# Kernel tuning notes

Hardware: AMD Instinct MI355X
Metric: run time of the kernel (lower is better)

Reference implementation:

```python
import jax, jax.numpy as jnp
import numpy as np
import math

B, N, DEG, C, F0, NCLS = 128, 512, 8, 128, 128, 10
E = B * N * DEG
RATIO = 0.8
K1 = math.ceil(RATIO * N)    # 410
K2 = math.ceil(RATIO * K1)   # 328
K3 = math.ceil(RATIO * K2)   # 263


def setup_inputs() -> dict:
    key = jax.random.key(0)
    ks = jax.random.split(key, 32)
    x = jax.random.normal(ks[0], (B * N, F0), jnp.float32)
    epg = N * DEG
    src_l = jax.random.randint(ks[1], (B, epg), 0, N)
    dst_l = jax.random.randint(ks[2], (B, epg), 0, N)
    off = (jnp.arange(B, dtype=jnp.int32) * N)[:, None]
    edge_src = (src_l + off).reshape(-1).astype(jnp.int32)
    edge_dst = (dst_l + off).reshape(-1).astype(jnp.int32)

    def lin(k, fi, fo):
        return jax.random.normal(k, (fi, fo), jnp.float32) / np.float32(np.sqrt(fi))

    inp = {"x": x, "edge_src": edge_src, "edge_dst": edge_dst}
    i = 3
    for s, fi in (("1", F0), ("2", C), ("3", C)):
        inp["Wroot" + s] = lin(ks[i], fi, C); i += 1
        inp["Wrel" + s] = lin(ks[i], fi, C); i += 1
        inp["brel" + s] = jnp.zeros((C,), jnp.float32)
        inp["p" + s] = jax.random.normal(ks[i], (C,), jnp.float32); i += 1
    inp["W1"] = lin(ks[i], 2 * C, 128); i += 1
    inp["b1"] = jnp.zeros((128,), jnp.float32)
    inp["W2"] = lin(ks[i], 128, 64); i += 1
    inp["b2"] = jnp.zeros((64,), jnp.float32)
    inp["W3"] = lin(ks[i], 64, NCLS); i += 1
    inp["b3"] = jnp.zeros((NCLS,), jnp.float32)
    return inp


def graph_conv(x, src, dst, emask, Wroot, Wrel, brel, num_nodes):
    # PyG GraphConv (aggr='add'): lin_rel(sum_j x_j) + lin_root(x_i)
    msg = x[src] * emask[:, None]                      # masked gather  [E, C]
    agg = jax.ops.segment_sum(msg, dst, num_segments=num_nodes)
    return agg @ Wrel + brel + x @ Wroot


def topk_pool(x, p, src, dst, emask, b, n, k):
    # score = tanh(x . p / ||p||), keep top-k nodes per graph, scale kept x by score
    score = jnp.tanh((x @ p) / jnp.linalg.norm(p))     # [b*n]
    vals, idx = jax.lax.top_k(score.reshape(b, n), k)  # [b, k]
    perm = (idx + (jnp.arange(b, dtype=idx.dtype) * n)[:, None]).reshape(-1)
    x_new = x[perm] * vals.reshape(-1, 1)
    inv = jnp.full((b * n,), -1, jnp.int32).at[perm].set(
        jnp.arange(b * k, dtype=jnp.int32))
    ns, nd = inv[src], inv[dst]
    nmask = emask * (ns >= 0) * (nd >= 0)
    return x_new, jnp.maximum(ns, 0), jnp.maximum(nd, 0), nmask


def readout(h, b, k):
    hb = h.reshape(b, k, -1)
    return jnp.concatenate([hb.max(axis=1), hb.mean(axis=1)], axis=-1)  # gmp||gap


def reference(x, edge_src, edge_dst,
              Wroot1, Wrel1, brel1, p1,
              Wroot2, Wrel2, brel2, p2,
              Wroot3, Wrel3, brel3, p3,
              W1, b1, W2, b2, W3, b3):
    emask = jnp.ones((E,), x.dtype)
    s, d = edge_src, edge_dst

    h = jax.nn.relu(graph_conv(x, s, d, emask, Wroot1, Wrel1, brel1, B * N))
    h, s, d, emask = topk_pool(h, p1, s, d, emask, B, N, K1)
    x1 = readout(h, B, K1)

    h = jax.nn.relu(graph_conv(h, s, d, emask, Wroot2, Wrel2, brel2, B * K1))
    h, s, d, emask = topk_pool(h, p2, s, d, emask, B, K1, K2)
    x2 = readout(h, B, K2)

    h = jax.nn.relu(graph_conv(h, s, d, emask, Wroot3, Wrel3, brel3, B * K2))
    h, s, d, emask = topk_pool(h, p3, s, d, emask, B, K2, K3)
    x3 = readout(h, B, K3)

    g = x1 + x2 + x3                                   # [B, 256]
    g = jax.nn.relu(g @ W1 + b1)                       # dropout is identity in eval
    g = jax.nn.relu(g @ W2 + b2)
    return jax.nn.log_softmax(g @ W3 + b3, axis=-1)    # [B, NCLS]
```

## Files before the change

### kernel.cpp

```cpp
#include <hip/hip_runtime.h>
#include <hip/hip_bf16.h>
#include <math.h>

#define B_G   128
#define N0    512
#define DEG   8
#define CCH   128
#define EPG   (N0*DEG)
#define E_TOTAL (B_G*EPG)
#define K1    410
#define K2    328
#define K3    263
#define NCLS  10

using bf16x8 = __attribute__((ext_vector_type(8))) __bf16;
using f32x4  = __attribute__((ext_vector_type(4))) float;
typedef unsigned short ushort;
typedef unsigned int uint;
typedef unsigned long long u64;

__device__ __forceinline__ ushort f2b(float f) {
    uint u = __float_as_uint(f);
    u += 0x7fffu + ((u >> 16) & 1u);
    return (ushort)(u >> 16);
}
__device__ __forceinline__ float b2f(ushort h) {
    return __uint_as_float(((uint)h) << 16);
}
__device__ __forceinline__ void split2(float v, ushort& hi, ushort& lo) {
    hi = f2b(v);
    lo = f2b(v - b2f(hi));
}
__device__ __forceinline__ uint pksplit(float v) {
    ushort h, l; split2(v, h, l);
    return (uint)h | ((uint)l << 16);
}
__device__ __forceinline__ float unpk(uint u) {
    return __uint_as_float(u << 16) + __uint_as_float(u & 0xffff0000u);
}
__device__ __forceinline__ float keyval(u64 key) {
    uint tu = (uint)(key >> 32);
    uint su = (tu & 0x80000000u) ? (tu & 0x7fffffffu) : ~tu;
    return __uint_as_float(su);
}

__global__ __launch_bounds__(512) void setup_kernel(
        const float* __restrict__ Wrel0, const float* __restrict__ Wroot0,
        const float* __restrict__ Wrel1, const float* __restrict__ Wroot1,
        const float* __restrict__ Wrel2, const float* __restrict__ Wroot2,
        ushort* __restrict__ Bph, ushort* __restrict__ Bpl,
        const int* __restrict__ es, const int* __restrict__ ed,
        int* __restrict__ indptr0, int* __restrict__ counts0, ushort* __restrict__ srclist0) {
    __shared__ uint epk[EPG];
    __shared__ int cnt[512], pref[512], curs[512];
    if (blockIdx.x < B_G) {
        int b = blockIdx.x, tid = threadIdx.x;
        cnt[tid] = 0;
        __syncthreads();
        int base = b * EPG;
        for (int i = tid; i < EPG; i += 512) {
            int s = es[base + i] & (N0 - 1);
            int d = ed[base + i] & (N0 - 1);
            epk[i] = (uint)s | ((uint)d << 16);
            atomicAdd(&cnt[d], 1);
        }
        __syncthreads();
        pref[tid] = cnt[tid];
        __syncthreads();
        for (int off = 1; off < 512; off <<= 1) {
            int v = (tid >= off) ? pref[tid - off] : 0;
            __syncthreads();
            pref[tid] += v;
            __syncthreads();
        }
        int excl = tid ? pref[tid - 1] : 0;
        indptr0[b * N0 + tid] = base + excl;
        counts0[b * N0 + tid] = cnt[tid];
        curs[tid] = excl;
        __syncthreads();
        for (int i = tid; i < EPG; i += 512) {
            uint wv = epk[i];
            int dl = wv >> 16;
            int pos = atomicAdd(&curs[dl], 1);
            srclist0[base + pos] = (ushort)(wv & 0xFFFFu);
        }
    } else {
        int i = (blockIdx.x - B_G) * 512 + threadIdx.x;
        if (i < 3 * 32768) {
            int layer = i >> 15, rem = i & 32767;
            int j = rem & 7, lane = (rem >> 3) & 63, cf = (rem >> 9) & 7, ks = rem >> 12;
            int k = ks * 32 + (lane >> 4) * 8 + j;
            int c = cf * 16 + (lane & 15);
            const float* Wrel  = layer == 0 ? Wrel0  : layer == 1 ? Wrel1  : Wrel2;
            const float* Wroot = layer == 0 ? Wroot0 : layer == 1 ? Wroot1 : Wroot2;
            float v = (k < 128) ? Wrel[k * 128 + c] : Wroot[(k - 128) * 128 + c];
            ushort hi, lo; split2(v, hi, lo);
            Bph[i] = hi; Bpl[i] = lo;
        }
    }
}

__global__ __launch_bounds__(1024) void aggregate0(
        const float* __restrict__ xf,
        const int* __restrict__ indptr, const int* __restrict__ counts,
        const ushort* __restrict__ srclist,
        uint* __restrict__ aggp) {
    extern __shared__ float slab[];
    int b = blockIdx.x >> 2, q = blockIdx.x & 3;
    int tid = threadIdx.x;
    const float4* xf4 = (const float4*)xf;
    for (int t = tid; t < N0 * 8; t += 1024) {
        int nd = t >> 3, c4 = t & 7;
        float4 u = xf4[(size_t)(b * N0 + nd) * 32 + q * 8 + c4];
        *(float4*)&slab[nd * 32 + c4 * 4] = u;
    }
    __syncthreads();
    int wave = tid >> 6, lane = tid & 63;
    int gl = lane >> 3, sub = lane & 7;
    for (int g = wave; g < N0 / 8; g += 16) {
        int d = g * 8 + gl;
        int beg = indptr[b * N0 + d];
        int cnt = counts[b * N0 + d];
        float4 acc = make_float4(0.f, 0.f, 0.f, 0.f);
        int id_next = (cnt > 0) ? (int)srclist[beg] : 0;
        for (int j = 0; j < cnt; j++) {
            int id = id_next;
            if (j + 1 < cnt) id_next = (int)srclist[beg + j + 1];
            const float4 v = *(const float4*)&slab[id * 32 + sub * 4];
            acc.x += v.x; acc.y += v.y; acc.z += v.z; acc.w += v.w;
        }
        uint4 o;
        o.x = pksplit(acc.x); o.y = pksplit(acc.y);
        o.z = pksplit(acc.z); o.w = pksplit(acc.w);
        *(uint4*)&aggp[(size_t)(b * N0 + d) * CCH + q * 32 + sub * 4] = o;
    }
}

__global__ __launch_bounds__(512, 4) void transform_mfma(
        const uint* __restrict__ aggp, const uint* __restrict__ hin,
        const float* __restrict__ rootf,
        const int* __restrict__ perm, const float* __restrict__ pval,
        const ushort* __restrict__ Bph, const ushort* __restrict__ Bpl,
        const float* __restrict__ brel, const float* __restrict__ pvec,
        uint* __restrict__ hout, float* __restrict__ score) {
    __shared__ ushort ldsBh[16384];
    __shared__ ushort ldsBl[16384];
    int tid = threadIdx.x;
    int wave = tid >> 6, lane = tid & 63;
    int r = lane & 15, kb = lane >> 4;
    int rows0 = blockIdx.x * 128 + wave * 16;
    int gid = rows0 + r;
    size_t oldrow = perm ? (size_t)perm[gid] : (size_t)gid;
    float rv = perm ? pval[gid] : 1.f;

    f32x4 acc[8];
#pragma unroll
    for (int cf = 0; cf < 8; cf++) acc[cf] = (f32x4)(0.f);

    union U16 { uint u[4]; bf16x8 v; };

#pragma unroll
    for (int half = 0; half < 2; half++) {
        if (half) __syncthreads();
#pragma unroll
        for (int i = 0; i < 4; i++) {
            int idx = tid + i * 512;
            ((uint4*)ldsBh)[idx] = ((const uint4*)(Bph + half * 16384))[idx];
            ((uint4*)ldsBl)[idx] = ((const uint4*)(Bpl + half * 16384))[idx];
        }
        __syncthreads();
#pragma unroll
        for (int ks4 = 0; ks4 < 4; ks4++) {
            U16 ah, al;
            if (half && rootf) {
                const float* R = rootf + (size_t)gid * CCH + ks4 * 32 + kb * 8;
                float4 f0 = *(const float4*)R;
                float4 f1 = *(const float4*)(R + 4);
                float c[8] = {f0.x, f0.y, f0.z, f0.w, f1.x, f1.y, f1.z, f1.w};
#pragma unroll
                for (int p2 = 0; p2 < 4; p2++) {
                    ushort h0, l0, h1, l1;
                    split2(c[2 * p2], h0, l0);
                    split2(c[2 * p2 + 1], h1, l1);
                    ah.u[p2] = (uint)h0 | ((uint)h1 << 16);
                    al.u[p2] = (uint)l0 | ((uint)l1 << 16);
                }
            } else {
                const uint* A = half ? hin : aggp;
                size_t abase = half ? oldrow * CCH : (size_t)gid * CCH;
                size_t rowbase = abase + ks4 * 32 + kb * 8;
                uint4 ua = *(const uint4*)&A[rowbase];
                uint4 ub = *(const uint4*)&A[rowbase + 4];
                if (half && perm) {
                    float c[8] = {unpk(ua.x) * rv, unpk(ua.y) * rv, unpk(ua.z) * rv,
                                  unpk(ua.w) * rv, unpk(ub.x) * rv, unpk(ub.y) * rv,
                                  unpk(ub.z) * rv, unpk(ub.w) * rv};
#pragma unroll
                    for (int p2 = 0; p2 < 4; p2++) {
                        ushort h0, l0, h1, l1;
                        split2(c[2 * p2], h0, l0);
                        split2(c[2 * p2 + 1], h1, l1);
                        ah.u[p2] = (uint)h0 | ((uint)h1 << 16);
                        al.u[p2] = (uint)l0 | ((uint)l1 << 16);
                    }
                } else {
                    ah.u[0] = (ua.x & 0xffffu) | (ua.y << 16);
                    ah.u[1] = (ua.z & 0xffffu) | (ua.w << 16);
                    ah.u[2] = (ub.x & 0xffffu) | (ub.y << 16);
                    ah.u[3] = (ub.z & 0xffffu) | (ub.w << 16);
                    al.u[0] = (ua.x >> 16) | (ua.y & 0xffff0000u);
                    al.u[1] = (ua.z >> 16) | (ua.w & 0xffff0000u);
                    al.u[2] = (ub.x >> 16) | (ub.y & 0xffff0000u);
                    al.u[3] = (ub.z >> 16) | (ub.w & 0xffff0000u);
                }
            }
#pragma unroll
            for (int cf = 0; cf < 8; cf++) {
                bf16x8 bh = *(const bf16x8*)&ldsBh[((ks4 * 8 + cf) * 64 + lane) * 8];
                bf16x8 bl = *(const bf16x8*)&ldsBl[((ks4 * 8 + cf) * 64 + lane) * 8];
                acc[cf] = __builtin_amdgcn_mfma_f32_16x16x32_bf16(ah.v, bl, acc[cf], 0, 0, 0);
                acc[cf] = __builtin_amdgcn_mfma_f32_16x16x32_bf16(al.v, bh, acc[cf], 0, 0, 0);
                acc[cf] = __builtin_amdgcn_mfma_f32_16x16x32_bf16(ah.v, bh, acc[cf], 0, 0, 0);
            }
        }
    }

    float pv[8], bb[8], q = 0.f;
#pragma unroll
    for (int cf = 0; cf < 8; cf++) {
        pv[cf] = pvec[cf * 16 + r];
        bb[cf] = brel[cf * 16 + r];
        q += pv[cf] * pv[cf];
    }
    float dots[4] = {0.f, 0.f, 0.f, 0.f};
#pragma unroll
    for (int cf = 0; cf < 8; cf++) {
#pragma unroll
        for (int reg = 0; reg < 4; reg++) {
            float v = acc[cf][reg] + bb[cf];
            v = v > 0.f ? v : 0.f;
            hout[(size_t)(rows0 + kb * 4 + reg) * CCH + cf * 16 + r] = pksplit(v);
            dots[reg] += v * pv[cf];
        }
    }
#pragma unroll
    for (int off = 1; off < 16; off <<= 1) {
        q += __shfl_xor(q, off);
#pragma unroll
        for (int reg = 0; reg < 4; reg++) dots[reg] += __shfl_xor(dots[reg], off);
    }
    if (r == 0) {
        float inv_norm = rsqrtf(q);
#pragma unroll
        for (int reg = 0; reg < 4; reg++)
            score[rows0 + kb * 4 + reg] = tanhf(dots[reg] * inv_norm);
    }
}

__global__ __launch_bounds__(1024) void poolagg_kernel(
        const float* __restrict__ score, const uint* __restrict__ hp,
        int* __restrict__ perm_out, float* __restrict__ pval_out,
        float* __restrict__ gpart,
        const int* __restrict__ ipt_in, const int* __restrict__ cnt_in,
        const ushort* __restrict__ src_in,
        int* __restrict__ ipt_out, int* __restrict__ cnt_out,
        ushort* __restrict__ src_out,
        uint* __restrict__ aggout,
        int n, int k, int do_agg) {
    int b = blockIdx.x >> 2, q = blockIdx.x & 3;
    int tid = threadIdx.x;
    __shared__ u64 keys[512];
    __shared__ short invl[512];
    __shared__ int prefL[512];
    __shared__ int wtot[8], woff[8];
    __shared__ ushort srcIn[EPG];
    __shared__ float wredbuf[2048];
    ushort* srcOut = (ushort*)wredbuf;
    extern __shared__ float slab[];

    u64 key = 0ull;
    if (tid < n) {
        uint u = __float_as_uint(score[b * n + tid]);
        u = (u & 0x80000000u) ? ~u : (u | 0x80000000u);
        key = ((u64)u << 32) | (uint)(~tid);
    }
    if (tid < 512) invl[tid] = -1;
    if (do_agg) {
        const uint* s4 = (const uint*)(src_in + b * EPG);
        uint* d4 = (uint*)srcIn;
        for (int i = tid; i < EPG / 2; i += 1024) d4[i] = s4[i];
    }
    for (int kk2 = 2; kk2 <= 512; kk2 <<= 1) {
        for (int j = kk2 >> 1; j > 0; j >>= 1) {
            if (j >= 64) {
                if (tid < 512) keys[tid] = key;
                __syncthreads();
                if (tid < 512) {
                    u64 p = keys[tid ^ j];
                    bool desc = ((tid & kk2) == 0);
                    bool lower = ((tid & j) == 0);
                    u64 mx = key > p ? key : p;
                    u64 mn = key > p ? p : key;
                    key = (desc == lower) ? mx : mn;
                }
                __syncthreads();
            } else if (tid < 512) {
                u64 p = __shfl_xor(key, j);
                bool desc = ((tid & kk2) == 0);
                bool lower = ((tid & j) == 0);
                u64 mx = key > p ? key : p;
                u64 mn = key > p ? p : key;
                key = (desc == lower) ? mx : mn;
            }
        }
    }
    if (tid < 512) keys[tid] = key;
    __syncthreads();
    if (tid < k) {
        int node = (int)(~(uint)key);
        invl[node] = (short)tid;
    }
    __syncthreads();
    for (int t = tid; t < k * 8; t += 1024) {
        int nd = t >> 3, c4 = t & 7;
        u64 kk = keys[nd];
        int node = (int)(~(uint)kk);
        float v = keyval(kk);
        uint4 u = *(const uint4*)&hp[(size_t)(b * n + node) * CCH + q * 32 + c4 * 4];
        *(float4*)&slab[nd * 32 + c4 * 4] =
            make_float4(unpk(u.x) * v, unpk(u.y) * v, unpk(u.z) * v, unpk(u.w) * v);
    }
    __syncthreads();
    {
        int w = tid >> 5, ch = tid & 31;
        float mx = -1e30f, sm = 0.f;
        for (int r2 = w; r2 < k; r2 += 32) {
            float v = slab[r2 * 32 + ch];
            mx = fmaxf(mx, v); sm += v;
        }
        wredbuf[w * 32 + ch] = mx;
        wredbuf[1024 + w * 32 + ch] = sm;
    }
    __syncthreads();
    if (tid < 32) {
        float m = -1e30f, s = 0.f;
        for (int w = 0; w < 32; w++) {
            m = fmaxf(m, wredbuf[w * 32 + tid]);
            s += wredbuf[1024 + w * 32 + tid];
        }
        gpart[b * 256 + q * 32 + tid] = m;
        gpart[b * 256 + 128 + q * 32 + tid] = s / (float)k;
    }
    if (!do_agg) return;
    __syncthreads();
    int node = -1, beg = 0, c = 0, nk = 0;
    if (tid < k) {
        node = (int)(~(uint)key);
        beg = ipt_in[b * n + node] - b * EPG;
        c = cnt_in[b * n + node];
        for (int t = 0; t < c; t++)
            if (invl[srcIn[beg + t]] >= 0) nk++;
    }
    {
        int lane = tid & 63;
        int v = (tid < k) ? nk : 0;
        int incl = v;
#pragma unroll
        for (int o = 1; o < 64; o <<= 1) {
            int t = __shfl_up(incl, o);
            if (lane >= o) incl += t;
        }
        if (tid < 512 && lane == 63) wtot[tid >> 6] = incl;
        __syncthreads();
        if (tid < 8) {
            int s = 0;
            for (int w = 0; w < tid; w++) s += wtot[w];
            woff[tid] = s;
        }
        __syncthreads();
        if (tid < 512) prefL[tid] = incl + woff[tid >> 6];
        __syncthreads();
    }
    int excl = (tid < 512 && tid) ? prefL[tid - 1] : 0;
    if (tid < k) {
        int pos = excl;
        for (int t = 0; t < c; t++) {
            int ns = invl[srcIn[beg + t]];
            if (ns >= 0) srcOut[pos++] = (ushort)ns;
        }
    }
    __syncthreads();
    if (q == 0) {
        int tot = prefL[511];
        if (tid < k) {
            ipt_out[b * k + tid] = b * EPG + excl;
            cnt_out[b * k + tid] = nk;
            perm_out[b * k + tid] = b * n + node;
            pval_out[b * k + tid] = keyval(key);
        }
        for (int i = tid; i < tot; i += 1024) src_out[b * EPG + i] = srcOut[i];
    }
    {
        int wave = tid >> 6, lane = tid & 63;
        int gl = lane >> 3, sub = lane & 7;
        int ngroups = (k + 7) >> 3;
        for (int g = wave; g < ngroups; g += 16) {
            int d = g * 8 + gl;
            bool act = d < k;
            int bg = 0, en = 0;
            if (act) { bg = d ? prefL[d - 1] : 0; en = prefL[d]; }
            int cc = en - bg;
            float4 acc = make_float4(0.f, 0.f, 0.f, 0.f);
            int id_next = (cc > 0) ? (int)srcOut[bg] : 0;
            for (int j = 0; j < cc; j++) {
                int id = id_next;
                if (j + 1 < cc) id_next = (int)srcOut[bg + j + 1];
                const float4 v = *(const float4*)&slab[id * 32 + sub * 4];
                acc.x += v.x; acc.y += v.y; acc.z += v.z; acc.w += v.w;
            }
            if (act) {
                uint4 o;
                o.x = pksplit(acc.x); o.y = pksplit(acc.y);
                o.z = pksplit(acc.z); o.w = pksplit(acc.w);
                *(uint4*)&aggout[(size_t)(b * k + d) * CCH + q * 32 + sub * 4] = o;
            }
        }
    }
}

__global__ __launch_bounds__(128) void mlp_kernel(const float* __restrict__ gpart,
        const float* __restrict__ W1, const float* __restrict__ b1,
        const float* __restrict__ W2, const float* __restrict__ b2,
        const float* __restrict__ W3, const float* __restrict__ b3,
        float* __restrict__ out) {
    int b = blockIdx.x, t = threadIdx.x;
    __shared__ float gs[256], h1[128], h2[64], lg[10];
    const float* g0 = gpart + ((size_t)0 * B_G + b) * 256;
    const float* g1 = gpart + ((size_t)1 * B_G + b) * 256;
    const float* g2 = gpart + ((size_t)2 * B_G + b) * 256;
    gs[t] = g0[t] + g1[t] + g2[t];
    gs[128 + t] = g0[128 + t] + g1[128 + t] + g2[128 + t];
    __syncthreads();
    {
        float a = b1[t];
        for (int c = 0; c < 256; c++) a += gs[c] * W1[c * 128 + t];
        h1[t] = fmaxf(a, 0.f);
    }
    __syncthreads();
    if (t < 64) {
        float a = b2[t];
        for (int c = 0; c < 128; c++) a += h1[c] * W2[c * 64 + t];
        h2[t] = fmaxf(a, 0.f);
    }
    __syncthreads();
    if (t < 10) {
        float a = b3[t];
        for (int c = 0; c < 64; c++) a += h2[c] * W3[c * 10 + t];
        lg[t] = a;
    }
    __syncthreads();
    if (t < 10) {
        float m = lg[0];
        for (int i = 1; i < 10; i++) m = fmaxf(m, lg[i]);
        float s = 0.f;
        for (int i = 0; i < 10; i++) s += expf(lg[i] - m);
        out[b * 10 + t] = lg[t] - m - logf(s);
    }
}

extern "C" void kernel_launch(void* const* d_in, const int* in_sizes, int n_in,
                              void* d_out, int out_size, void* d_ws, size_t ws_size,
                              hipStream_t stream) {
    (void)in_sizes; (void)n_in; (void)out_size; (void)ws_size;
    const float* x0 = (const float*)d_in[0];
    const int* es = (const int*)d_in[1];
    const int* ed = (const int*)d_in[2];
    const float* Wroot[3] = {(const float*)d_in[3], (const float*)d_in[7], (const float*)d_in[11]};
    const float* Wrel[3]  = {(const float*)d_in[4], (const float*)d_in[8], (const float*)d_in[12]};
    const float* brel[3]  = {(const float*)d_in[5], (const float*)d_in[9], (const float*)d_in[13]};
    const float* pvec[3]  = {(const float*)d_in[6], (const float*)d_in[10], (const float*)d_in[14]};
    const float* W1 = (const float*)d_in[15];
    const float* b1 = (const float*)d_in[16];
    const float* W2 = (const float*)d_in[17];
    const float* b2 = (const float*)d_in[18];
    const float* W3 = (const float*)d_in[19];
    const float* b3 = (const float*)d_in[20];

    size_t off = 0;
    char* base = (char*)d_ws;
    auto alloc = [&](size_t bytes) -> void* {
        void* p = base + off;
        off += (bytes + 255) & ~(size_t)255;
        return p;
    };
    const size_t FEATP = (size_t)(B_G * N0) * CCH * 4;
    uint* P0 = (uint*)alloc(FEATP);
    uint* P1 = (uint*)alloc(FEATP);
    uint* P2 = (uint*)alloc(FEATP);
    ushort* Bph = (ushort*)alloc((size_t)3 * 32768 * 2);
    ushort* Bpl = (ushort*)alloc((size_t)3 * 32768 * 2);
    int* iptA = (int*)alloc((size_t)(B_G * N0) * 4);
    int* cntA = (int*)alloc((size_t)(B_G * N0) * 4);
    ushort* srcA = (ushort*)alloc((size_t)E_TOTAL * 2);
    int* iptB = (int*)alloc((size_t)(B_G * N0) * 4);
    int* cntB = (int*)alloc((size_t)(B_G * N0) * 4);
    ushort* srcB = (ushort*)alloc((size_t)E_TOTAL * 2);
    int* permA = (int*)alloc((size_t)(B_G * K1) * 4);
    float* pvalA = (float*)alloc((size_t)(B_G * K1) * 4);
    int* permB = (int*)alloc((size_t)(B_G * K1) * 4);
    float* pvalB = (float*)alloc((size_t)(B_G * K1) * 4);
    float* score = (float*)alloc((size_t)(B_G * N0) * 4);
    float* gpart = (float*)alloc((size_t)3 * B_G * 256 * 4);

    setup_kernel<<<B_G + (3 * 32768 + 511) / 512, 512, 0, stream>>>(
        Wrel[0], Wroot[0], Wrel[1], Wroot[1], Wrel[2], Wroot[2],
        Bph, Bpl, es, ed, iptA, cntA, srcA);

    aggregate0<<<4 * B_G, 1024, (size_t)N0 * 32 * 4, stream>>>(
        x0, iptA, cntA, srcA, P1);
    transform_mfma<<<B_G * N0 / 128, 512, 0, stream>>>(
        P1, nullptr, x0, nullptr, nullptr, Bph, Bpl, brel[0], pvec[0], P0, score);
    poolagg_kernel<<<4 * B_G, 1024, (size_t)K1 * 32 * 4, stream>>>(
        score, P0, permA, pvalA, gpart + (size_t)0 * B_G * 256,
        iptA, cntA, srcA, iptB, cntB, srcB, P1, N0, K1, 1);

    transform_mfma<<<B_G * K1 / 128, 512, 0, stream>>>(
        P1, P0, nullptr, permA, pvalA, Bph + 32768, Bpl + 32768,
        brel[1], pvec[1], P2, score);
    poolagg_kernel<<<4 * B_G, 1024, (size_t)K2 * 32 * 4, stream>>>(
        score, P2, permB, pvalB, gpart + (size_t)1 * B_G * 256,
        iptB, cntB, srcB, iptA, cntA, srcA, P1, K1, K2, 1);

    transform_mfma<<<B_G * K2 / 128, 512, 0, stream>>>(
        P1, P2, nullptr, permB, pvalB, Bph + 2 * 32768, Bpl + 2 * 32768,
        brel[2], pvec[2], P0, score);
    poolagg_kernel<<<4 * B_G, 1024, (size_t)K3 * 32 * 4, stream>>>(
        score, P0, nullptr, nullptr, gpart + (size_t)2 * B_G * 256,
        iptA, cntA, srcA, nullptr, nullptr, nullptr, nullptr, K2, K3, 0);

    mlp_kernel<<<B_G, 128, 0, stream>>>(gpart, W1, b1, W2, b2, W3, b3, (float*)d_out);
}
```

Measured before the change: 196.5 us.

## Split pooling into per-graph sort kernel and per-quarter aggregation; swizzle LDS slab

The fused pool kernel ran the bitonic top-k sort and CSR compaction redundantly in each of the four channel-quarter blocks per graph. This splits it into a pool_sort kernel (one 512-thread block per graph, doing the sort, perm/pval output and edge-list compaction once) and a pool_agg kernel (four blocks per graph, doing gather, readout and neighbour aggregation from the compacted CSR). It also XOR-swizzles the float4 layout of the LDS feature slab to reduce bank conflicts in the random-row gathers. The cost is three extra launches and a round-trip of perm/pval/CSR through global memory.

```diff
diff --git a/kernel.cpp b/kernel.cpp
--- a/kernel.cpp
+++ b/kernel.cpp
@@ -12,6 +12,8 @@
 #define K2    328
 #define K3    263
 #define NCLS  10
+
+#define SWZ(row, cb) ((((cb) ^ ((row) & 7)) << 2))
 
 using bf16x8 = __attribute__((ext_vector_type(8))) __bf16;
 using f32x4  = __attribute__((ext_vector_type(4))) float;
@@ -112,7 +114,7 @@
     for (int t = tid; t < N0 * 8; t += 1024) {
         int nd = t >> 3, c4 = t & 7;
         float4 u = xf4[(size_t)(b * N0 + nd) * 32 + q * 8 + c4];
-        *(float4*)&slab[nd * 32 + c4 * 4] = u;
+        *(float4*)&slab[nd * 32 + SWZ(nd, c4)] = u;
     }
     __syncthreads();
     int wave = tid >> 6, lane = tid & 63;
@@ -126,7 +128,7 @@
         for (int j = 0; j < cnt; j++) {
             int id = id_next;
             if (j + 1 < cnt) id_next = (int)srclist[beg + j + 1];
-            const float4 v = *(const float4*)&slab[id * 32 + sub * 4];
+            const float4 v = *(const float4*)&slab[id * 32 + SWZ(id, sub)];
             acc.x += v.x; acc.y += v.y; acc.z += v.z; acc.w += v.w;
         }
         uint4 o;
@@ -257,26 +259,21 @@
     }
 }
 
-__global__ __launch_bounds__(1024) void poolagg_kernel(
-        const float* __restrict__ score, const uint* __restrict__ hp,
+__global__ __launch_bounds__(512) void pool_sort(
+        const float* __restrict__ score,
         int* __restrict__ perm_out, float* __restrict__ pval_out,
-        float* __restrict__ gpart,
         const int* __restrict__ ipt_in, const int* __restrict__ cnt_in,
         const ushort* __restrict__ src_in,
         int* __restrict__ ipt_out, int* __restrict__ cnt_out,
         ushort* __restrict__ src_out,
-        uint* __restrict__ aggout,
-        int n, int k, int do_agg) {
-    int b = blockIdx.x >> 2, q = blockIdx.x & 3;
-    int tid = threadIdx.x;
+        int n, int k, int do_csr) {
+    int b = blockIdx.x, tid = threadIdx.x;
     __shared__ u64 keys[512];
     __shared__ short invl[512];
     __shared__ int prefL[512];
     __shared__ int wtot[8], woff[8];
     __shared__ ushort srcIn[EPG];
-    __shared__ float wredbuf[2048];
-    ushort* srcOut = (ushort*)wredbuf;
-    extern __shared__ float slab[];
+    __shared__ ushort srcOut[EPG];
 
     u64 key = 0ull;
     if (tid < n) {
@@ -284,27 +281,25 @@
         u = (u & 0x80000000u) ? ~u : (u | 0x80000000u);
         key = ((u64)u << 32) | (uint)(~tid);
     }
-    if (tid < 512) invl[tid] = -1;
-    if (do_agg) {
+    invl[tid] = -1;
+    if (do_csr) {
         const uint* s4 = (const uint*)(src_in + b * EPG);
         uint* d4 = (uint*)srcIn;
-        for (int i = tid; i < EPG / 2; i += 1024) d4[i] = s4[i];
+        for (int i = tid; i < EPG / 2; i += 512) d4[i] = s4[i];
     }
     for (int kk2 = 2; kk2 <= 512; kk2 <<= 1) {
         for (int j = kk2 >> 1; j > 0; j >>= 1) {
             if (j >= 64) {
-                if (tid < 512) keys[tid] = key;
+                keys[tid] = key;
                 __syncthreads();
-                if (tid < 512) {
-                    u64 p = keys[tid ^ j];
-                    bool desc = ((tid & kk2) == 0);
-                    bool lower = ((tid & j) == 0);
-                    u64 mx = key > p ? key : p;
-                    u64 mn = key > p ? p : key;
-                    key = (desc == lower) ? mx : mn;
-                }
+                u64 p = keys[tid ^ j];
+                bool desc = ((tid & kk2) == 0);
+                bool lower = ((tid & j) == 0);
+                u64 mx = key > p ? key : p;
+                u64 mn = key > p ? p : key;
+                key = (desc == lower) ? mx : mn;
                 __syncthreads();
-            } else if (tid < 512) {
+            } else {
                 u64 p = __shfl_xor(key, j);
                 bool desc = ((tid & kk2) == 0);
                 bool lower = ((tid & j) == 0);
@@ -314,20 +309,81 @@
             }
         }
     }
-    if (tid < 512) keys[tid] = key;
-    __syncthreads();
+    int node = (int)(~(uint)key);
     if (tid < k) {
-        int node = (int)(~(uint)key);
         invl[node] = (short)tid;
-    }
-    __syncthreads();
+        perm_out[b * k + tid] = b * n + node;
+        pval_out[b * k + tid] = keyval(key);
+    }
+    if (!do_csr) return;
+    __syncthreads();
+    int beg = 0, c = 0, nk = 0;
+    if (tid < k) {
+        beg = ipt_in[b * n + node] - b * EPG;
+        c = cnt_in[b * n + node];
+        for (int t = 0; t < c; t++)
+            if (invl[srcIn[beg + t]] >= 0) nk++;
+    }
+    {
+        int lane = tid & 63;
+        int incl = (tid < k) ? nk : 0;
+#pragma unroll
+        for (int o = 1; o < 64; o <<= 1) {
+            int t = __shfl_up(incl, o);
+            if (lane >= o) incl += t;
+        }
+        if (lane == 63) wtot[tid >> 6] = incl;
+        __syncthreads();
+        if (tid < 8) {
+            int s = 0;
+            for (int w = 0; w < tid; w++) s += wtot[w];
+            woff[tid] = s;
+        }
+        __syncthreads();
+        prefL[tid] = incl + woff[tid >> 6];
+        __syncthreads();
+    }
+    int excl = tid ? prefL[tid - 1] : 0;
+    if (tid < k) {
+        ipt_out[b * k + tid] = b * EPG + excl;
+        cnt_out[b * k + tid] = nk;
+        int pos = excl;
+        for (int t = 0; t < c; t++) {
+            int ns = invl[srcIn[beg + t]];
+            if (ns >= 0) srcOut[pos++] = (ushort)ns;
+        }
+    }
+    __syncthreads();
+    int tot = prefL[511];
+    for (int i = tid; i < tot; i += 512) src_out[b * EPG + i] = srcOut[i];
+}
+
+__global__ __launch_bounds__(1024) void pool_agg(
+        const uint* __restrict__ hp,
+        const int* __restrict__ perm, const float* __restrict__ pval,
+        float* __restrict__ gpart,
+        const int* __restrict__ ipt, const int* __restrict__ cnt,
+        const ushort* __restrict__ srcl,
+        uint* __restrict__ aggout,
+        int n, int k, int do_agg) {
+    int b = blockIdx.x >> 2, q = blockIdx.x & 3;
+    int tid = threadIdx.x;
+    __shared__ ushort srcL[EPG];
+    __shared__ float redbuf[2048];
+    extern __shared__ float slab[];
+
+    if (do_agg) {
+        int tot = (ipt[b * k + k - 1] - b * EPG) + cnt[b * k + k - 1];
+        const uint* s4 = (const uint*)(srcl + b * EPG);
+        uint* d4 = (uint*)srcL;
+        for (int i = tid; i < (tot + 1) / 2; i += 1024) d4[i] = s4[i];
+    }
     for (int t = tid; t < k * 8; t += 1024) {
         int nd = t >> 3, c4 = t & 7;
-        u64 kk = keys[nd];
-        int node = (int)(~(uint)kk);
-        float v = keyval(kk);
-        uint4 u = *(const uint4*)&hp[(size_t)(b * n + node) * CCH + q * 32 + c4 * 4];
-        *(float4*)&slab[nd * 32 + c4 * 4] =
+        size_t old = (size_t)perm[b * k + nd];
+        float v = pval[b * k + nd];
+        uint4 u = *(const uint4*)&hp[old * CCH + q * 32 + c4 * 4];
+        *(float4*)&slab[nd * 32 + SWZ(nd, c4)] =
             make_float4(unpk(u.x) * v, unpk(u.y) * v, unpk(u.z) * v, unpk(u.w) * v);
     }
     __syncthreads();
@@ -335,71 +391,23 @@
         int w = tid >> 5, ch = tid & 31;
         float mx = -1e30f, sm = 0.f;
         for (int r2 = w; r2 < k; r2 += 32) {
-            float v = slab[r2 * 32 + ch];
+            float v = slab[r2 * 32 + SWZ(r2, ch >> 2) + (ch & 3)];
             mx = fmaxf(mx, v); sm += v;
         }
-        wredbuf[w * 32 + ch] = mx;
-        wredbuf[1024 + w * 32 + ch] = sm;
+        redbuf[w * 32 + ch] = mx;
+        redbuf[1024 + w * 32 + ch] = sm;
     }
     __syncthreads();
     if (tid < 32) {
         float m = -1e30f, s = 0.f;
         for (int w = 0; w < 32; w++) {
-            m = fmaxf(m, wredbuf[w * 32 + tid]);
-            s += wredbuf[1024 + w * 32 + tid];
+            m = fmaxf(m, redbuf[w * 32 + tid]);
+            s += redbuf[1024 + w * 32 + tid];
         }
         gpart[b * 256 + q * 32 + tid] = m;
         gpart[b * 256 + 128 + q * 32 + tid] = s / (float)k;
     }
     if (!do_agg) return;
-    __syncthreads();
-    int node = -1, beg = 0, c = 0, nk = 0;
-    if (tid < k) {
-        node = (int)(~(uint)key);
-        beg = ipt_in[b * n + node] - b * EPG;
-        c = cnt_in[b * n + node];
-        for (int t = 0; t < c; t++)
-            if (invl[srcIn[beg + t]] >= 0) nk++;
-    }
-    {
-        int lane = tid & 63;
-        int v = (tid < k) ? nk : 0;
-        int incl = v;
-#pragma unroll
-        for (int o = 1; o < 64; o <<= 1) {
-            int t = __shfl_up(incl, o);
-            if (lane >= o) incl += t;
-        }
-        if (tid < 512 && lane == 63) wtot[tid >> 6] = incl;
-        __syncthreads();
-        if (tid < 8) {
-            int s = 0;
-            for (int w = 0; w < tid; w++) s += wtot[w];
-            woff[tid] = s;
-        }
-        __syncthreads();
-        if (tid < 512) prefL[tid] = incl + woff[tid >> 6];
-        __syncthreads();
-    }
-    int excl = (tid < 512 && tid) ? prefL[tid - 1] : 0;
-    if (tid < k) {
-        int pos = excl;
-        for (int t = 0; t < c; t++) {
-            int ns = invl[srcIn[beg + t]];
-            if (ns >= 0) srcOut[pos++] = (ushort)ns;
-        }
-    }
-    __syncthreads();
-    if (q == 0) {
-        int tot = prefL[511];
-        if (tid < k) {
-            ipt_out[b * k + tid] = b * EPG + excl;
-            cnt_out[b * k + tid] = nk;
-            perm_out[b * k + tid] = b * n + node;
-            pval_out[b * k + tid] = keyval(key);
-        }
-        for (int i = tid; i < tot; i += 1024) src_out[b * EPG + i] = srcOut[i];
-    }
     {
         int wave = tid >> 6, lane = tid & 63;
         int gl = lane >> 3, sub = lane & 7;
@@ -407,15 +415,14 @@
         for (int g = wave; g < ngroups; g += 16) {
             int d = g * 8 + gl;
             bool act = d < k;
-            int bg = 0, en = 0;
-            if (act) { bg = d ? prefL[d - 1] : 0; en = prefL[d]; }
-            int cc = en - bg;
+            int bg = 0, cc = 0;
+            if (act) { bg = ipt[b * k + d] - b * EPG; cc = cnt[b * k + d]; }
             float4 acc = make_float4(0.f, 0.f, 0.f, 0.f);
-            int id_next = (cc > 0) ? (int)srcOut[bg] : 0;
+            int id_next = (cc > 0) ? (int)srcL[bg] : 0;
             for (int j = 0; j < cc; j++) {
                 int id = id_next;
-                if (j + 1 < cc) id_next = (int)srcOut[bg + j + 1];
-                const float4 v = *(const float4*)&slab[id * 32 + sub * 4];
+                if (j + 1 < cc) id_next = (int)srcL[bg + j + 1];
+                const float4 v = *(const float4*)&slab[id * 32 + SWZ(id, sub)];
                 acc.x += v.x; acc.y += v.y; acc.z += v.z; acc.w += v.w;
             }
             if (act) {
@@ -520,23 +527,29 @@
         x0, iptA, cntA, srcA, P1);
     transform_mfma<<<B_G * N0 / 128, 512, 0, stream>>>(
         P1, nullptr, x0, nullptr, nullptr, Bph, Bpl, brel[0], pvec[0], P0, score);
-    poolagg_kernel<<<4 * B_G, 1024, (size_t)K1 * 32 * 4, stream>>>(
-        score, P0, permA, pvalA, gpart + (size_t)0 * B_G * 256,
-        iptA, cntA, srcA, iptB, cntB, srcB, P1, N0, K1, 1);
+    pool_sort<<<B_G, 512, 0, stream>>>(
+        score, permA, pvalA, iptA, cntA, srcA, iptB, cntB, srcB, N0, K1, 1);
+    pool_agg<<<4 * B_G, 1024, (size_t)K1 * 32 * 4, stream>>>(
+        P0, permA, pvalA, gpart + (size_t)0 * B_G * 256,
+        iptB, cntB, srcB, P1, N0, K1, 1);
 
     transform_mfma<<<B_G * K1 / 128, 512, 0, stream>>>(
         P1, P0, nullptr, permA, pvalA, Bph + 32768, Bpl + 32768,
         brel[1], pvec[1], P2, score);
-    poolagg_kernel<<<4 * B_G, 1024, (size_t)K2 * 32 * 4, stream>>>(
-        score, P2, permB, pvalB, gpart + (size_t)1 * B_G * 256,
-        iptB, cntB, srcB, iptA, cntA, srcA, P1, K1, K2, 1);
+    pool_sort<<<B_G, 512, 0, stream>>>(
+        score, permB, pvalB, iptB, cntB, srcB, iptA, cntA, srcA, K1, K2, 1);
+    pool_agg<<<4 * B_G, 1024, (size_t)K2 * 32 * 4, stream>>>(
+        P2, permB, pvalB, gpart + (size_t)1 * B_G * 256,
+        iptA, cntA, srcA, P1, K1, K2, 1);
 
     transform_mfma<<<B_G * K2 / 128, 512, 0, stream>>>(
         P1, P2, nullptr, permB, pvalB, Bph + 2 * 32768, Bpl + 2 * 32768,
         brel[2], pvec[2], P0, score);
-    poolagg_kernel<<<4 * B_G, 1024, (size_t)K3 * 32 * 4, stream>>>(
-        score, P0, nullptr, nullptr, gpart + (size_t)2 * B_G * 256,
-        iptA, cntA, srcA, nullptr, nullptr, nullptr, nullptr, K2, K3, 0);
+    pool_sort<<<B_G, 512, 0, stream>>>(
+        score, permA, pvalA, nullptr, nullptr, nullptr, nullptr, nullptr, nullptr, K2, K3, 0);
+    pool_agg<<<4 * B_G, 1024, (size_t)K3 * 32 * 4, stream>>>(
+        P0, permA, pvalA, gpart + (size_t)2 * B_G * 256,
+        nullptr, nullptr, nullptr, nullptr, K2, K3, 0);
 
     mlp_kernel<<<B_G, 128, 0, stream>>>(gpart, W1, b1, W2, b2, W3, b3, (float*)d_out);
 }
```

Measured after the change: 200.9 us. +2.2%, slower.

## Restructure pooling: overlap feature load with sort, write pooled features, swizzle LDS

Applied to the files above, without the earlier changes.

The pool kernel now has threads 512-1023 load all n node features into a swizzled LDS slab while threads 0-511 run the first bitonic stages in registers with shuffles. It scales kept rows in place, writes the pooled features to a dense buffer, and aggregates by reading the original edge list and filtering through the inverse map, instead of first building a compacted edge list in LDS. Edge compaction for the next layer is done only by the q==0 block, and transform_mfma loses its perm/pval gather-and-resplit path because it now reads a pre-pooled root matrix. The costs are a larger LDS slab (n rows instead of k), an extra global write of pooled features, and divergent filter checks inside the aggregation loop.

```diff
diff --git a/kernel.cpp b/kernel.cpp
--- a/kernel.cpp
+++ b/kernel.cpp
@@ -12,6 +12,8 @@
 #define K2    328
 #define K3    263
 #define NCLS  10
+
+#define SWZ(row, cb) ((((cb) ^ ((row) & 7)) << 2))
 
 using bf16x8 = __attribute__((ext_vector_type(8))) __bf16;
 using f32x4  = __attribute__((ext_vector_type(4))) float;
@@ -112,7 +114,7 @@
     for (int t = tid; t < N0 * 8; t += 1024) {
         int nd = t >> 3, c4 = t & 7;
         float4 u = xf4[(size_t)(b * N0 + nd) * 32 + q * 8 + c4];
-        *(float4*)&slab[nd * 32 + c4 * 4] = u;
+        *(float4*)&slab[nd * 32 + SWZ(nd, c4)] = u;
     }
     __syncthreads();
     int wave = tid >> 6, lane = tid & 63;
@@ -126,7 +128,7 @@
         for (int j = 0; j < cnt; j++) {
             int id = id_next;
             if (j + 1 < cnt) id_next = (int)srclist[beg + j + 1];
-            const float4 v = *(const float4*)&slab[id * 32 + sub * 4];
+            const float4 v = *(const float4*)&slab[id * 32 + SWZ(id, sub)];
             acc.x += v.x; acc.y += v.y; acc.z += v.z; acc.w += v.w;
         }
         uint4 o;
@@ -137,9 +139,8 @@
 }
 
 __global__ __launch_bounds__(512, 4) void transform_mfma(
-        const uint* __restrict__ aggp, const uint* __restrict__ hin,
+        const uint* __restrict__ aggp, const uint* __restrict__ rootp,
         const float* __restrict__ rootf,
-        const int* __restrict__ perm, const float* __restrict__ pval,
         const ushort* __restrict__ Bph, const ushort* __restrict__ Bpl,
         const float* __restrict__ brel, const float* __restrict__ pvec,
         uint* __restrict__ hout, float* __restrict__ score) {
@@ -150,8 +151,6 @@
     int r = lane & 15, kb = lane >> 4;
     int rows0 = blockIdx.x * 128 + wave * 16;
     int gid = rows0 + r;
-    size_t oldrow = perm ? (size_t)perm[gid] : (size_t)gid;
-    float rv = perm ? pval[gid] : 1.f;
 
     f32x4 acc[8];
 #pragma unroll
@@ -186,33 +185,18 @@
                     al.u[p2] = (uint)l0 | ((uint)l1 << 16);
                 }
             } else {
-                const uint* A = half ? hin : aggp;
-                size_t abase = half ? oldrow * CCH : (size_t)gid * CCH;
-                size_t rowbase = abase + ks4 * 32 + kb * 8;
+                const uint* A = half ? rootp : aggp;
+                size_t rowbase = (size_t)gid * CCH + ks4 * 32 + kb * 8;
                 uint4 ua = *(const uint4*)&A[rowbase];
                 uint4 ub = *(const uint4*)&A[rowbase + 4];
-                if (half && perm) {
-                    float c[8] = {unpk(ua.x) * rv, unpk(ua.y) * rv, unpk(ua.z) * rv,
-                                  unpk(ua.w) * rv, unpk(ub.x) * rv, unpk(ub.y) * rv,
-                                  unpk(ub.z) * rv, unpk(ub.w) * rv};
-#pragma unroll
-                    for (int p2 = 0; p2 < 4; p2++) {
-                        ushort h0, l0, h1, l1;
-                        split2(c[2 * p2], h0, l0);
-                        split2(c[2 * p2 + 1], h1, l1);
-                        ah.u[p2] = (uint)h0 | ((uint)h1 << 16);
-                        al.u[p2] = (uint)l0 | ((uint)l1 << 16);
-                    }
-                } else {
-                    ah.u[0] = (ua.x & 0xffffu) | (ua.y << 16);
-                    ah.u[1] = (ua.z & 0xffffu) | (ua.w << 16);
-                    ah.u[2] = (ub.x & 0xffffu) | (ub.y << 16);
-                    ah.u[3] = (ub.z & 0xffffu) | (ub.w << 16);
-                    al.u[0] = (ua.x >> 16) | (ua.y & 0xffff0000u);
-                    al.u[1] = (ua.z >> 16) | (ua.w & 0xffff0000u);
-                    al.u[2] = (ub.x >> 16) | (ub.y & 0xffff0000u);
-                    al.u[3] = (ub.z >> 16) | (ub.w & 0xffff0000u);
-                }
+                ah.u[0] = (ua.x & 0xffffu) | (ua.y << 16);
+                ah.u[1] = (ua.z & 0xffffu) | (ua.w << 16);
+                ah.u[2] = (ub.x & 0xffffu) | (ub.y << 16);
+                ah.u[3] = (ub.z & 0xffffu) | (ub.w << 16);
+                al.u[0] = (ua.x >> 16) | (ua.y & 0xffff0000u);
+                al.u[1] = (ua.z >> 16) | (ua.w & 0xffff0000u);
+                al.u[2] = (ub.x >> 16) | (ub.y & 0xffff0000u);
+                al.u[3] = (ub.z >> 16) | (ub.w & 0xffff0000u);
             }
 #pragma unroll
             for (int cf = 0; cf < 8; cf++) {
@@ -257,40 +241,52 @@
     }
 }
 
-__global__ __launch_bounds__(1024) void poolagg_kernel(
+__global__ __launch_bounds__(1024) void pool_kernel(
         const float* __restrict__ score, const uint* __restrict__ hp,
-        int* __restrict__ perm_out, float* __restrict__ pval_out,
         float* __restrict__ gpart,
         const int* __restrict__ ipt_in, const int* __restrict__ cnt_in,
         const ushort* __restrict__ src_in,
         int* __restrict__ ipt_out, int* __restrict__ cnt_out,
         ushort* __restrict__ src_out,
-        uint* __restrict__ aggout,
-        int n, int k, int do_agg) {
+        uint* __restrict__ pooledX, uint* __restrict__ aggout,
+        int n, int k, int do_next) {
     int b = blockIdx.x >> 2, q = blockIdx.x & 3;
     int tid = threadIdx.x;
     __shared__ u64 keys[512];
     __shared__ short invl[512];
+    __shared__ float redbuf[1024];
     __shared__ int prefL[512];
     __shared__ int wtot[8], woff[8];
-    __shared__ ushort srcIn[EPG];
-    __shared__ float wredbuf[2048];
-    ushort* srcOut = (ushort*)wredbuf;
     extern __shared__ float slab[];
 
     u64 key = 0ull;
-    if (tid < n) {
-        uint u = __float_as_uint(score[b * n + tid]);
-        u = (u & 0x80000000u) ? ~u : (u | 0x80000000u);
-        key = ((u64)u << 32) | (uint)(~tid);
-    }
-    if (tid < 512) invl[tid] = -1;
-    if (do_agg) {
-        const uint* s4 = (const uint*)(src_in + b * EPG);
-        uint* d4 = (uint*)srcIn;
-        for (int i = tid; i < EPG / 2; i += 1024) d4[i] = s4[i];
-    }
-    for (int kk2 = 2; kk2 <= 512; kk2 <<= 1) {
+    if (tid < 512) {
+        if (tid < n) {
+            uint u = __float_as_uint(score[b * n + tid]);
+            u = (u & 0x80000000u) ? ~u : (u | 0x80000000u);
+            key = ((u64)u << 32) | (uint)(~tid);
+        }
+        invl[tid] = -1;
+        for (int kk2 = 2; kk2 <= 64; kk2 <<= 1) {
+            for (int j = kk2 >> 1; j > 0; j >>= 1) {
+                u64 p = __shfl_xor(key, j);
+                bool desc = ((tid & kk2) == 0);
+                bool lower = ((tid & j) == 0);
+                u64 mx = key > p ? key : p;
+                u64 mn = key > p ? p : key;
+                key = (desc == lower) ? mx : mn;
+            }
+        }
+    } else {
+        for (int t = tid - 512; t < n * 8; t += 512) {
+            int nd = t >> 3, c4 = t & 7;
+            uint4 u = *(const uint4*)&hp[(size_t)(b * n + nd) * CCH + q * 32 + c4 * 4];
+            *(float4*)&slab[nd * 32 + SWZ(nd, c4)] =
+                make_float4(unpk(u.x), unpk(u.y), unpk(u.z), unpk(u.w));
+        }
+    }
+    __syncthreads();
+    for (int kk2 = 128; kk2 <= 512; kk2 <<= 1) {
         for (int j = kk2 >> 1; j > 0; j >>= 1) {
             if (j >= 64) {
                 if (tid < 512) keys[tid] = key;
@@ -316,89 +312,47 @@
     }
     if (tid < 512) keys[tid] = key;
     __syncthreads();
-    if (tid < k) {
-        int node = (int)(~(uint)key);
-        invl[node] = (short)tid;
-    }
+    if (tid < k) invl[(int)(~(uint)key)] = (short)tid;
     __syncthreads();
     for (int t = tid; t < k * 8; t += 1024) {
-        int nd = t >> 3, c4 = t & 7;
-        u64 kk = keys[nd];
-        int node = (int)(~(uint)kk);
+        int rank = t >> 3, c4 = t & 7;
+        u64 kk = keys[rank];
+        int old = (int)(~(uint)kk);
         float v = keyval(kk);
-        uint4 u = *(const uint4*)&hp[(size_t)(b * n + node) * CCH + q * 32 + c4 * 4];
-        *(float4*)&slab[nd * 32 + c4 * 4] =
-            make_float4(unpk(u.x) * v, unpk(u.y) * v, unpk(u.z) * v, unpk(u.w) * v);
-    }
-    __syncthreads();
-    {
+        float* p = &slab[old * 32 + SWZ(old, c4)];
+        p[0] *= v; p[1] *= v; p[2] *= v; p[3] *= v;
+    }
+    __syncthreads();
+    if (tid < 512) {
         int w = tid >> 5, ch = tid & 31;
         float mx = -1e30f, sm = 0.f;
-        for (int r2 = w; r2 < k; r2 += 32) {
-            float v = slab[r2 * 32 + ch];
+        for (int r2 = w; r2 < k; r2 += 16) {
+            int old = (int)(~(uint)keys[r2]);
+            float v = slab[old * 32 + SWZ(old, ch >> 2) + (ch & 3)];
             mx = fmaxf(mx, v); sm += v;
         }
-        wredbuf[w * 32 + ch] = mx;
-        wredbuf[1024 + w * 32 + ch] = sm;
+        redbuf[w * 32 + ch] = mx;
+        redbuf[512 + w * 32 + ch] = sm;
     }
     __syncthreads();
     if (tid < 32) {
         float m = -1e30f, s = 0.f;
-        for (int w = 0; w < 32; w++) {
-            m = fmaxf(m, wredbuf[w * 32 + tid]);
-            s += wredbuf[1024 + w * 32 + tid];
+        for (int w = 0; w < 16; w++) {
+            m = fmaxf(m, redbuf[w * 32 + tid]);
+            s += redbuf[512 + w * 32 + tid];
         }
         gpart[b * 256 + q * 32 + tid] = m;
         gpart[b * 256 + 128 + q * 32 + tid] = s / (float)k;
     }
-    if (!do_agg) return;
-    __syncthreads();
-    int node = -1, beg = 0, c = 0, nk = 0;
-    if (tid < k) {
-        node = (int)(~(uint)key);
-        beg = ipt_in[b * n + node] - b * EPG;
-        c = cnt_in[b * n + node];
-        for (int t = 0; t < c; t++)
-            if (invl[srcIn[beg + t]] >= 0) nk++;
-    }
-    {
-        int lane = tid & 63;
-        int v = (tid < k) ? nk : 0;
-        int incl = v;
-#pragma unroll
-        for (int o = 1; o < 64; o <<= 1) {
-            int t = __shfl_up(incl, o);
-            if (lane >= o) incl += t;
-        }
-        if (tid < 512 && lane == 63) wtot[tid >> 6] = incl;
-        __syncthreads();
-        if (tid < 8) {
-            int s = 0;
-            for (int w = 0; w < tid; w++) s += wtot[w];
-            woff[tid] = s;
-        }
-        __syncthreads();
-        if (tid < 512) prefL[tid] = incl + woff[tid >> 6];
-        __syncthreads();
-    }
-    int excl = (tid < 512 && tid) ? prefL[tid - 1] : 0;
-    if (tid < k) {
-        int pos = excl;
-        for (int t = 0; t < c; t++) {
-            int ns = invl[srcIn[beg + t]];
-            if (ns >= 0) srcOut[pos++] = (ushort)ns;
-        }
-    }
-    __syncthreads();
-    if (q == 0) {
-        int tot = prefL[511];
-        if (tid < k) {
-            ipt_out[b * k + tid] = b * EPG + excl;
-            cnt_out[b * k + tid] = nk;
-            perm_out[b * k + tid] = b * n + node;
-            pval_out[b * k + tid] = keyval(key);
-        }
-        for (int i = tid; i < tot; i += 1024) src_out[b * EPG + i] = srcOut[i];
+    if (!do_next) return;
+    for (int t = tid; t < k * 8; t += 1024) {
+        int rank = t >> 3, c4 = t & 7;
+        int old = (int)(~(uint)keys[rank]);
+        const float* p = &slab[old * 32 + SWZ(old, c4)];
+        uint4 o;
+        o.x = pksplit(p[0]); o.y = pksplit(p[1]);
+        o.z = pksplit(p[2]); o.w = pksplit(p[3]);
+        *(uint4*)&pooledX[(size_t)(b * k + rank) * CCH + q * 32 + c4 * 4] = o;
     }
     {
         int wave = tid >> 6, lane = tid & 63;
@@ -407,22 +361,64 @@
         for (int g = wave; g < ngroups; g += 16) {
             int d = g * 8 + gl;
             bool act = d < k;
-            int bg = 0, en = 0;
-            if (act) { bg = d ? prefL[d - 1] : 0; en = prefL[d]; }
-            int cc = en - bg;
+            int beg = 0, cc = 0;
+            if (act) {
+                int old = (int)(~(uint)keys[d]);
+                beg = ipt_in[b * n + old];
+                cc = cnt_in[b * n + old];
+            }
             float4 acc = make_float4(0.f, 0.f, 0.f, 0.f);
-            int id_next = (cc > 0) ? (int)srcOut[bg] : 0;
+            int s_next = (cc > 0) ? (int)src_in[beg] : 0;
             for (int j = 0; j < cc; j++) {
-                int id = id_next;
-                if (j + 1 < cc) id_next = (int)srcOut[bg + j + 1];
-                const float4 v = *(const float4*)&slab[id * 32 + sub * 4];
-                acc.x += v.x; acc.y += v.y; acc.z += v.z; acc.w += v.w;
+                int s = s_next;
+                if (j + 1 < cc) s_next = (int)src_in[beg + j + 1];
+                if (invl[s] >= 0) {
+                    const float4 v = *(const float4*)&slab[s * 32 + SWZ(s, sub)];
+                    acc.x += v.x; acc.y += v.y; acc.z += v.z; acc.w += v.w;
+                }
             }
             if (act) {
                 uint4 o;
                 o.x = pksplit(acc.x); o.y = pksplit(acc.y);
                 o.z = pksplit(acc.z); o.w = pksplit(acc.w);
                 *(uint4*)&aggout[(size_t)(b * k + d) * CCH + q * 32 + sub * 4] = o;
+            }
+        }
+    }
+    if (q == 0) {
+        int beg = 0, c = 0, nk = 0;
+        if (tid < k) {
+            int old = (int)(~(uint)keys[tid]);
+            beg = ipt_in[b * n + old];
+            c = cnt_in[b * n + old];
+            for (int t = 0; t < c; t++)
+                if (invl[src_in[beg + t]] >= 0) nk++;
+        }
+        int lane = tid & 63;
+        int incl = (tid < 512 && tid < k) ? nk : 0;
+#pragma unroll
+        for (int o = 1; o < 64; o <<= 1) {
+            int t = __shfl_up(incl, o);
+            if (lane >= o) incl += t;
+        }
+        if (tid < 512 && lane == 63) wtot[tid >> 6] = incl;
+        __syncthreads();
+        if (tid < 8) {
+            int s = 0;
+            for (int w = 0; w < tid; w++) s += wtot[w];
+            woff[tid] = s;
+        }
+        __syncthreads();
+        if (tid < 512) prefL[tid] = incl + woff[tid >> 6];
+        __syncthreads();
+        if (tid < k) {
+            int excl = tid ? prefL[tid - 1] : 0;
+            ipt_out[b * k + tid] = b * EPG + excl;
+            cnt_out[b * k + tid] = nk;
+            int pos = b * EPG + excl;
+            for (int t = 0; t < c; t++) {
+                int ns = invl[src_in[beg + t]];
+                if (ns >= 0) src_out[pos++] = (ushort)ns;
             }
         }
     }
@@ -505,10 +501,6 @@
     int* iptB = (int*)alloc((size_t)(B_G * N0) * 4);
     int* cntB = (int*)alloc((size_t)(B_G * N0) * 4);
     ushort* srcB = (ushort*)alloc((size_t)E_TOTAL * 2);
-    int* permA = (int*)alloc((size_t)(B_G * K1) * 4);
-    float* pvalA = (float*)alloc((size_t)(B_G * K1) * 4);
-    int* permB = (int*)alloc((size_t)(B_G * K1) * 4);
-    float* pvalB = (float*)alloc((size_t)(B_G * K1) * 4);
     float* score = (float*)alloc((size_t)(B_G * N0) * 4);
     float* gpart = (float*)alloc((size_t)3 * B_G * 256 * 4);
 
@@ -519,24 +511,22 @@
     aggregate0<<<4 * B_G, 1024, (size_t)N0 * 32 * 4, stream>>>(
         x0, iptA, cntA, srcA, P1);
     transform_mfma<<<B_G * N0 / 128, 512, 0, stream>>>(
-        P1, nullptr, x0, nullptr, nullptr, Bph, Bpl, brel[0], pvec[0], P0, score);
-    poolagg_kernel<<<4 * B_G, 1024, (size_t)K1 * 32 * 4, stream>>>(
-        score, P0, permA, pvalA, gpart + (size_t)0 * B_G * 256,
-        iptA, cntA, srcA, iptB, cntB, srcB, P1, N0, K1, 1);
+        P1, nullptr, x0, Bph, Bpl, brel[0], pvec[0], P0, score);
+    pool_kernel<<<4 * B_G, 1024, (size_t)N0 * 32 * 4, stream>>>(
+        score, P0, gpart + (size_t)0 * B_G * 256,
+        iptA, cntA, srcA, iptB, cntB, srcB, P2, P1, N0, K1, 1);
 
     transform_mfma<<<B_G * K1 / 128, 512, 0, stream>>>(
-        P1, P0, nullptr, permA, pvalA, Bph + 32768, Bpl + 32768,
-        brel[1], pvec[1], P2, score);
-    poolagg_kernel<<<4 * B_G, 1024, (size_t)K2 * 32 * 4, stream>>>(
-        score, P2, permB, pvalB, gpart + (size_t)1 * B_G * 256,
-        iptB, cntB, srcB, iptA, cntA, srcA, P1, K1, K2, 1);
+        P1, P2, nullptr, Bph + 32768, Bpl + 32768, brel[1], pvec[1], P0, score);
+    pool_kernel<<<4 * B_G, 1024, (size_t)K1 * 32 * 4, stream>>>(
+        score, P0, gpart + (size_t)1 * B_G * 256,
+        iptB, cntB, srcB, iptA, cntA, srcA, P2, P1, K1, K2, 1);
 
     transform_mfma<<<B_G * K2 / 128, 512, 0, stream>>>(
-        P1, P2, nullptr, permB, pvalB, Bph + 2 * 32768, Bpl + 2 * 32768,
-        brel[2], pvec[2], P0, score);
-    poolagg_kernel<<<4 * B_G, 1024, (size_t)K3 * 32 * 4, stream>>>(
-        score, P0, nullptr, nullptr, gpart + (size_t)2 * B_G * 256,
-        iptA, cntA, srcA, nullptr, nullptr, nullptr, nullptr, K2, K3, 0);
+        P1, P2, nullptr, Bph + 2 * 32768, Bpl + 2 * 32768, brel[2], pvec[2], P0, score);
+    pool_kernel<<<4 * B_G, 1024, (size_t)K2 * 32 * 4, stream>>>(
+        score, P0, gpart + (size_t)2 * B_G * 256,
+        iptA, cntA, srcA, nullptr, nullptr, nullptr, nullptr, nullptr, K2, K3, 0);
 
     mlp_kernel<<<B_G, 128, 0, stream>>>(gpart, W1, b1, W2, b2, W3, b3, (float*)d_out);
 }
```

Result: no change. 197.8 us (+0.6%).
